# Performance work log

Measured on AMD Instinct MI355X. Metric: run time of the kernel, lower is better.

## Reference

```python
import jax, jax.numpy as jnp
import numpy as np

N_HEADS = 16
EMBED_DIM = 1024
HEAD_DIM = EMBED_DIM // N_HEADS
SRC_LEN = 128  # diagonal offset of the tril mask
B, T = 2, 2048


def setup_inputs() -> dict:
    key = jax.random.key(0)
    ks = jax.random.split(key, 7)
    s = 0.02
    return {
        "x": jax.random.normal(ks[0], (B, T, EMBED_DIM), dtype=jnp.float32),
        "Wq": jax.random.normal(ks[1], (EMBED_DIM, EMBED_DIM), dtype=jnp.float32) * s,
        "bq": jax.random.normal(ks[2], (EMBED_DIM,), dtype=jnp.float32) * s,
        "Wk": jax.random.normal(ks[3], (EMBED_DIM, EMBED_DIM), dtype=jnp.float32) * s,
        "bk": jax.random.normal(ks[4], (EMBED_DIM,), dtype=jnp.float32) * s,
        "Wv": jax.random.normal(ks[5], (EMBED_DIM, EMBED_DIM), dtype=jnp.float32) * s,
        "bv": jax.random.normal(ks[6], (EMBED_DIM,), dtype=jnp.float32) * s,
    }


def reference(x, Wq, bq, Wk, bk, Wv, bv):
    b, t, c = x.shape
    # project and split heads: [B, H, T, Dh]
    def heads(w, bias):
        y = x @ w.T + bias
        return y.reshape(b, t, N_HEADS, HEAD_DIM).transpose(0, 2, 1, 3)

    q = heads(Wq, bq)
    k = heads(Wk, bk)
    v = heads(Wv, bv)

    scale = HEAD_DIM ** -0.5
    attn = jnp.einsum("bhqd,bhkd->bhqk", q, k) * scale  # [B,H,T,T]
    # prefix-causal mask: key j allowed iff j <= i + SRC_LEN
    i = jnp.arange(t)[:, None]
    j = jnp.arange(t)[None, :]
    mask = j <= i + SRC_LEN  # [T, T]
    attn = jnp.where(mask[None, None], attn, -jnp.inf)
    attn = jax.nn.softmax(attn, axis=-1)
    # dropout p=0.0 -> identity in eval/reference
    out = jnp.einsum("bhqk,bhkd->bhqd", attn, v)  # [B,H,T,Dh]
    return out.transpose(0, 2, 1, 3).reshape(b, t, c)
```

## Files before the change

### kernel.cpp

```cpp
#include <hip/hip_runtime.h>
#include <hip/hip_bf16.h>

#define B_    2
#define T_    2048
#define C_    1024
#define H_    16
#define D_    64
#define SRCL_ 128

typedef short  short8 __attribute__((ext_vector_type(8)));
typedef float  f32x4  __attribute__((ext_vector_type(4)));
typedef unsigned short ushort4_t __attribute__((ext_vector_type(4)));
typedef unsigned int   uint4v    __attribute__((ext_vector_type(4)));

#define QSCALE 0.18033688011112042f

__device__ inline unsigned short f2bf(float f) {
    union { float f; unsigned u; } v; v.f = f;
    unsigned r = v.u + 0x7FFFu + ((v.u >> 16) & 1u);
    return (unsigned short)(r >> 16);
}

#if __has_builtin(__builtin_amdgcn_exp2f)
#define EXP2F(x) __builtin_amdgcn_exp2f(x)
#else
#define EXP2F(x) exp2f(x)
#endif

__device__ __forceinline__ void async_ld16(const void* g, void* l) {
    __builtin_amdgcn_global_load_lds(
        (const __attribute__((address_space(1))) unsigned int*)g,
        (__attribute__((address_space(3))) unsigned int*)l, 16, 0, 0);
}

__global__ __launch_bounds__(256) void convert_all(
        const float* __restrict__ x,
        const float* __restrict__ wq,
        const float* __restrict__ wk,
        const float* __restrict__ wv,
        unsigned short* __restrict__ xb,
        unsigned short* __restrict__ wb)
{
    const int NX = (B_ * T_ * C_) / 4;
    const int NW = (C_ * C_) / 4;
    int i = blockIdx.x * 256 + threadIdx.x;
    const float4* src;
    ushort4_t* dst;
    if (i < NX)               { src = (const float4*)x;  dst = (ushort4_t*)xb;                }
    else if (i < NX + NW)     { src = (const float4*)wq; dst = (ushort4_t*)wb;                i -= NX; }
    else if (i < NX + 2*NW)   { src = (const float4*)wk; dst = (ushort4_t*)(wb + C_*C_);      i -= NX + NW; }
    else                      { src = (const float4*)wv; dst = (ushort4_t*)(wb + 2*C_*C_);    i -= NX + 2*NW; }
    float4 v = src[i];
    ushort4_t o;
    o.x = f2bf(v.x); o.y = f2bf(v.y); o.z = f2bf(v.z); o.w = f2bf(v.w);
    dst[i] = o;
}

__global__ __launch_bounds__(512, 2) void gemm_qkv(
        const unsigned short* __restrict__ xb,
        const unsigned short* __restrict__ wb,
        const float* __restrict__ bq,
        const float* __restrict__ bk,
        const float* __restrict__ bv,
        unsigned short* __restrict__ qo,
        unsigned short* __restrict__ ktp,
        unsigned short* __restrict__ vtp)
{
    __shared__ __align__(16) unsigned short uni[65536];

    const int tid  = threadIdx.x;
    const int wave = tid >> 6;
    const int lane = tid & 63;
    const int lane15 = lane & 15;
    const int quad   = lane >> 4;
    const int wm = wave >> 2;
    const int wn = wave & 3;

    const int bid = blockIdx.x;
    const int xcd = bid & 7;
    const int jj  = bid >> 3;
    const int mt  = xcd * 2 + (jj / 12);
    const int nt  = jj % 12;
    const int m0 = mt * 256;
    const int n0 = nt * 256;

    f32x4 acc[8][4];
#pragma unroll
    for (int m = 0; m < 8; ++m)
#pragma unroll
        for (int n = 0; n < 4; ++n)
            acc[m][n] = (f32x4){0.f, 0.f, 0.f, 0.f};

    char* lds = (char*)uni;
    const unsigned short* gb = (wave < 4) ? (xb + (size_t)m0 * 1024)
                                          : (wb + (size_t)n0 * 1024);
    const unsigned short* gsrc =
        gb + ((wave & 3) * 64 + (lane >> 2)) * 1024 + (lane & 3) * 8;
    const int lbase0 = ((wave < 4) ? 0 : 32768) + (wave & 3) * 4096;

    auto stage = [&](int t2, int kk) {
        char* ld = lds + (t2 & 1) * 65536 + lbase0 + kk * 16384;
        const unsigned short* gs = gsrc + t2 * 64 + kk * 32;
        async_ld16(gs,             ld);
        async_ld16(gs + 16 * 1024, ld + 1024);
        async_ld16(gs + 32 * 1024, ld + 2048);
        async_ld16(gs + 48 * 1024, ld + 3072);
    };

    auto compute = [&](int cur, int kk) {
        const char* ab = lds + cur * 65536 + kk * 16384;
        const char* bb = ab + 32768;
        short8 a[8], b[4];
#pragma unroll
        for (int n = 0; n < 4; ++n)
            b[n] = *(const short8*)(bb + (wn * 64 + n * 16 + lane15) * 64 + quad * 16);
#pragma unroll
        for (int m = 0; m < 8; ++m)
            a[m] = *(const short8*)(ab + (wm * 128 + m * 16 + lane15) * 64 + quad * 16);
#pragma unroll
        for (int m = 0; m < 8; ++m)
#pragma unroll
            for (int n = 0; n < 4; ++n)
                acc[m][n] = __builtin_amdgcn_mfma_f32_16x16x32_bf16(a[m], b[n], acc[m][n], 0, 0, 0);
    };

    stage(0, 0);
    stage(0, 1);

    for (int t = 0; t < 16; ++t) {
        const int cur = t & 1;
        __asm__ volatile("s_waitcnt vmcnt(4)\n\ts_barrier" ::: "memory");
        if (t < 15) stage(t + 1, 0);
        compute(cur, 0);
        if (t < 15) {
            __asm__ volatile("s_waitcnt vmcnt(4)\n\ts_barrier" ::: "memory");
            stage(t + 1, 1);
        } else {
            __asm__ volatile("s_waitcnt vmcnt(0)\n\ts_barrier" ::: "memory");
        }
        compute(cur, 1);
    }

    __syncthreads();

    const int colbase = n0 + wn * 64;
    const int which   = colbase >> 10;
    const int jj0     = colbase & 1023;
    const int h       = jj0 >> 6;
    const float* bias_p = (which == 0 ? bq : (which == 1 ? bk : bv)) + jj0;
    const float oscale  = (which == 0) ? QSCALE : 1.0f;

    unsigned short* stg = &uni[wave * 4160];

#pragma unroll
    for (int pass = 0; pass < 2; ++pass) {
        if (which != 2) {
#pragma unroll
            for (int ni = 0; ni < 4; ++ni) {
                const float bias = bias_p[ni * 16 + lane15];
                const int d = ni * 16 + lane15;
                const int dbase = (d >> 3) * 520 + (d & 7);
#pragma unroll
                for (int mi = 0; mi < 4; ++mi)
#pragma unroll
                    for (int r = 0; r < 4; ++r) {
                        const int tt = mi * 16 + quad * 4 + r;
                        stg[dbase + tt * 8] =
                            f2bf((acc[pass * 4 + mi][ni][r] + bias) * oscale);
                    }
            }
        } else {
#pragma unroll
            for (int ni = 0; ni < 4; ++ni) {
                const float bias = bias_p[ni * 16 + lane15];
                const int d = ni * 16 + lane15;
#pragma unroll
                for (int mi = 0; mi < 4; ++mi)
#pragma unroll
                    for (int r = 0; r < 4; ++r) {
                        const int tt = mi * 16 + quad * 4 + r;
                        const int c  = ((tt >> 5) << 2) | ((tt >> 2) & 3);
                        const int s  = (((tt >> 4) & 1) << 2) | (tt & 3);
                        stg[c * 520 + d * 8 + s] =
                            f2bf(acc[pass * 4 + mi][ni][r] + bias);
                    }
            }
        }

        const int rowg = m0 + wm * 128 + pass * 64;
        const int bidx = rowg >> 11;
        const int t0   = rowg & 2047;
        const size_t bh = (size_t)bidx * H_ + h;
        unsigned short* gdst =
            (which == 0 ? qo : (which == 1 ? ktp : vtp))
            + bh * (size_t)(T_ * D_) + (t0 >> 6) * 4096;

#pragma unroll
        for (int c = 0; c < 8; ++c) {
            *(short8*)&gdst[(c * 64 + lane) * 8] = *(const short8*)&stg[c * 520 + lane * 8];
        }
    }
}

__global__ __launch_bounds__(256, 4) void attn(
        const unsigned short* __restrict__ qg,
        const unsigned short* __restrict__ kg,
        const unsigned short* __restrict__ vg,
        float* __restrict__ out)
{
    __shared__ __align__(16) unsigned short stage[2][8192];

    const int tid  = threadIdx.x;
    const int wave = tid >> 6;
    const int lane = tid & 63;
    const int lane15 = lane & 15;
    const int quad   = lane >> 4;

    const int bh = blockIdx.x & 31;
    const int a  = 31 - (blockIdx.x >> 5);
    const int b  = bh >> 4;
    const int h  = bh & 15;
    const int i0 = a * 64 + wave * 16;

    const unsigned short* Q  = qg + (size_t)bh * T_ * D_;
    const unsigned short* KT = kg + (size_t)bh * T_ * D_;
    const unsigned short* VT = vg + (size_t)bh * T_ * D_;

    const int qrow = wave * 16 + lane15;
    const short8 qf0 = *(const short8*)&Q[a * 4096 + quad * 512 + qrow * 8];
    const short8 qf1 = *(const short8*)&Q[a * 4096 + (4 + quad) * 512 + qrow * 8];

    f32x4 o_acc[4];
#pragma unroll
    for (int di = 0; di < 4; ++di) o_acc[di] = (f32x4){0.f, 0.f, 0.f, 0.f};
    float l_p = 0.f;

    const int ntiles = min(a + 3, 32);
    const int limit  = i0 + lane15 + SRCL_;

    const int ib = wave * 4;
    const int loff = lane * 8;

#pragma unroll
    for (int c = 0; c < 4; ++c) {
        const int i = ib + c;
        const unsigned short* src = (i < 8) ? &KT[i * 512 + loff]
                                            : &VT[(i - 8) * 512 + loff];
        async_ld16(src, &stage[0][i * 512]);
    }

    for (int it = 0; it < ntiles; ++it) {
        __asm__ volatile("s_waitcnt vmcnt(0)\n\ts_barrier" ::: "memory");

        if (it + 1 < ntiles) {
            unsigned short* nb = &stage[(it + 1) & 1][0];
            const size_t tb = (size_t)(it + 1) * 4096;
#pragma unroll
            for (int c = 0; c < 4; ++c) {
                const int i = ib + c;
                const unsigned short* src = (i < 8) ? &KT[tb + i * 512 + loff]
                                                    : &VT[tb + (i - 8) * 512 + loff];
                async_ld16(src, &nb[i * 512]);
            }
        }

        const unsigned short* sb = &stage[it & 1][0];
        const int j0 = it << 6;

        f32x4 sv[4];
#pragma unroll
        for (int ni = 0; ni < 4; ++ni) {
            const short8 kf0 = *(const short8*)&sb[quad * 512 + (ni * 16 + lane15) * 8];
            const short8 kf1 = *(const short8*)&sb[(4 + quad) * 512 + (ni * 16 + lane15) * 8];
            f32x4 t = (f32x4){0.f, 0.f, 0.f, 0.f};
            t = __builtin_amdgcn_mfma_f32_16x16x32_bf16(kf0, qf0, t, 0, 0, 0);
            t = __builtin_amdgcn_mfma_f32_16x16x32_bf16(kf1, qf1, t, 0, 0, 0);
            sv[ni] = t;
        }

        if (j0 + 63 > i0 + SRCL_) {
#pragma unroll
            for (int ni = 0; ni < 4; ++ni)
#pragma unroll
                for (int r = 0; r < 4; ++r) {
                    const int key = j0 + ni * 16 + quad * 4 + r;
                    if (key > limit) sv[ni][r] = -INFINITY;
                }
        }

        float lacc = 0.f;
        unsigned pw[8];
#pragma unroll
        for (int ni = 0; ni < 4; ++ni) {
            const float p0 = EXP2F(sv[ni][0]);
            const float p1 = EXP2F(sv[ni][1]);
            const float p2 = EXP2F(sv[ni][2]);
            const float p3 = EXP2F(sv[ni][3]);
            lacc += (p0 + p1) + (p2 + p3);
            const unsigned u0 = __float_as_uint(p0) + 0x8000u;
            const unsigned u1 = __float_as_uint(p1) + 0x8000u;
            const unsigned u2 = __float_as_uint(p2) + 0x8000u;
            const unsigned u3 = __float_as_uint(p3) + 0x8000u;
            pw[ni * 2]     = __builtin_amdgcn_perm(u1, u0, 0x07060302);
            pw[ni * 2 + 1] = __builtin_amdgcn_perm(u3, u2, 0x07060302);
        }
        l_p += lacc;

        const uint4v w0 = {pw[0], pw[1], pw[2], pw[3]};
        const uint4v w1 = {pw[4], pw[5], pw[6], pw[7]};
        const short8 pf0 = __builtin_bit_cast(short8, w0);
        const short8 pf1 = __builtin_bit_cast(short8, w1);

#pragma unroll
        for (int di = 0; di < 4; ++di) {
            const short8 vf0 = *(const short8*)&sb[4096 + quad * 512 + (di * 16 + lane15) * 8];
            const short8 vf1 = *(const short8*)&sb[4096 + (4 + quad) * 512 + (di * 16 + lane15) * 8];
            o_acc[di] = __builtin_amdgcn_mfma_f32_16x16x32_bf16(vf0, pf0, o_acc[di], 0, 0, 0);
            o_acc[di] = __builtin_amdgcn_mfma_f32_16x16x32_bf16(vf1, pf1, o_acc[di], 0, 0, 0);
        }
    }

    __syncthreads();

    float l0s = l_p + __shfl_xor(l_p, 16);
    const float inv = 1.0f / (l0s + __shfl_xor(l0s, 32));

    float* myOs = (float*)&stage[0][0] + wave * 2048;
#pragma unroll
    for (int di = 0; di < 4; ++di) {
        f32x4 v = o_acc[di] * inv;
        *(f32x4*)&myOs[lane15 * 68 + di * 16 + quad * 4] = v;
    }
    float* orow0 = out + ((size_t)(b * T_ + i0)) * C_ + h * 64;
#pragma unroll
    for (int c = 0; c < 4; ++c) {
        const int idx = c * 64 + lane;
        const int t   = idx >> 4;
        const int dc  = (idx & 15) * 4;
        float4 v = *(float4*)&myOs[t * 68 + dc];
        *(float4*)(orow0 + (size_t)t * C_ + dc) = v;
    }
}

extern "C" void kernel_launch(void* const* d_in, const int* in_sizes, int n_in,
                              void* d_out, int out_size, void* d_ws, size_t ws_size,
                              hipStream_t stream) {
    const float* x  = (const float*)d_in[0];
    const float* Wq = (const float*)d_in[1];
    const float* bq = (const float*)d_in[2];
    const float* Wk = (const float*)d_in[3];
    const float* bk = (const float*)d_in[4];
    const float* Wv = (const float*)d_in[5];
    const float* bv = (const float*)d_in[6];
    float* out = (float*)d_out;

    unsigned short* xb  = (unsigned short*)d_ws;
    unsigned short* wb  = xb  + (size_t)B_ * T_ * C_;
    unsigned short* qb  = wb  + (size_t)3 * C_ * C_;
    unsigned short* ktb = qb  + (size_t)B_ * H_ * T_ * D_;
    unsigned short* vtb = ktb + (size_t)B_ * H_ * T_ * D_;

    convert_all<<<7168, 256, 0, stream>>>(x, Wq, Wk, Wv, xb, wb);
    gemm_qkv<<<192, 512, 0, stream>>>(xb, wb, bq, bk, bv, qb, ktb, vtb);
    attn<<<1024, 256, 0, stream>>>(qb, ktb, vtb, out);
}
```

Baseline: 145.4 us.

## Restructure QKV GEMM mainloop with finer-grained staging, LDS swizzle and setprio

Measured after the change: 144.1 us. About the same (-0.8%).

```diff
diff --git a/kernel.cpp b/kernel.cpp
--- a/kernel.cpp
+++ b/kernel.cpp
@@ -91,54 +91,63 @@
         for (int n = 0; n < 4; ++n)
             acc[m][n] = (f32x4){0.f, 0.f, 0.f, 0.f};
 
-    char* lds = (char*)uni;
-    const unsigned short* gb = (wave < 4) ? (xb + (size_t)m0 * 1024)
-                                          : (wb + (size_t)n0 * 1024);
-    const unsigned short* gsrc =
-        gb + ((wave & 3) * 64 + (lane >> 2)) * 1024 + (lane & 3) * 8;
-    const int lbase0 = ((wave < 4) ? 0 : 32768) + (wave & 3) * 4096;
-
-    auto stage = [&](int t2, int kk) {
-        char* ld = lds + (t2 & 1) * 65536 + lbase0 + kk * 16384;
-        const unsigned short* gs = gsrc + t2 * 64 + kk * 32;
-        async_ld16(gs,             ld);
-        async_ld16(gs + 16 * 1024, ld + 1024);
-        async_ld16(gs + 32 * 1024, ld + 2048);
-        async_ld16(gs + 48 * 1024, ld + 3072);
+    const int srow  = tid >> 2;
+    const int kseg8 = ((tid & 3) ^ ((tid >> 3) & 3)) * 8;
+    const unsigned short* gA = xb + (size_t)(m0 + srow) * 1024 + kseg8;
+    const unsigned short* gB = wb + (size_t)(n0 + srow) * 1024 + kseg8;
+    char* lbase = (char*)uni + tid * 16;
+
+    auto stage = [&](int s) {
+        const int Tt = s >> 2, j = s & 3;
+        const unsigned short* g = ((j & 1) ? gB : gA) + Tt * 64 + (j >> 1) * 32;
+        char* l = lbase + (Tt & 1) * 65536 + (j & 1) * 32768 + (j >> 1) * 16384;
+        async_ld16(g, l);
+        async_ld16(g + 128 * 1024, l + 8192);
     };
 
-    auto compute = [&](int cur, int kk) {
-        const char* ab = lds + cur * 65536 + kk * 16384;
-        const char* bb = ab + 32768;
-        short8 a[8], b[4];
-#pragma unroll
-        for (int n = 0; n < 4; ++n)
-            b[n] = *(const short8*)(bb + (wn * 64 + n * 16 + lane15) * 64 + quad * 16);
-#pragma unroll
-        for (int m = 0; m < 8; ++m)
-            a[m] = *(const short8*)(ab + (wm * 128 + m * 16 + lane15) * 64 + quad * 16);
-#pragma unroll
-        for (int m = 0; m < 8; ++m)
-#pragma unroll
-            for (int n = 0; n < 4; ++n)
-                acc[m][n] = __builtin_amdgcn_mfma_f32_16x16x32_bf16(a[m], b[n], acc[m][n], 0, 0, 0);
-    };
-
-    stage(0, 0);
-    stage(0, 1);
-
-    for (int t = 0; t < 16; ++t) {
-        const int cur = t & 1;
-        __asm__ volatile("s_waitcnt vmcnt(4)\n\ts_barrier" ::: "memory");
-        if (t < 15) stage(t + 1, 0);
-        compute(cur, 0);
-        if (t < 15) {
-            __asm__ volatile("s_waitcnt vmcnt(4)\n\ts_barrier" ::: "memory");
-            stage(t + 1, 1);
-        } else {
-            __asm__ volatile("s_waitcnt vmcnt(0)\n\ts_barrier" ::: "memory");
-        }
-        compute(cur, 1);
+#pragma unroll
+    for (int s = 0; s < 6; ++s) stage(s);
+    __asm__ volatile("s_waitcnt vmcnt(4)\n\ts_barrier" ::: "memory");
+
+    const int swz = (quad ^ ((lane15 >> 1) & 3)) * 16;
+
+    for (int T = 0; T < 16; ++T) {
+        const char* bufp = (const char*)uni + (T & 1) * 65536;
+        short8 bf[4];
+#pragma unroll
+        for (int ph = 0; ph < 4; ++ph) {
+            const int h = ph & 1, kk = ph >> 1;
+            const char* Ap = bufp + kk * 16384;
+            const char* Bp = bufp + 32768 + kk * 16384;
+
+            short8 a[4];
+#pragma unroll
+            for (int mi = 0; mi < 4; ++mi)
+                a[mi] = *(const short8*)(Ap + (wm * 128 + h * 64 + mi * 16 + lane15) * 64 + swz);
+            if (h == 0) {
+#pragma unroll
+                for (int ni = 0; ni < 4; ++ni)
+                    bf[ni] = *(const short8*)(Bp + (wn * 64 + ni * 16 + lane15) * 64 + swz);
+            }
+
+            const int s = T * 4 + ph + 6;
+            if (s < 64) stage(s);
+
+            __asm__ volatile("s_barrier" ::: "memory");
+            __builtin_amdgcn_s_setprio(1);
+#pragma unroll
+            for (int mi = 0; mi < 4; ++mi)
+#pragma unroll
+                for (int ni = 0; ni < 4; ++ni)
+                    acc[h * 4 + mi][ni] = __builtin_amdgcn_mfma_f32_16x16x32_bf16(
+                        a[mi], bf[ni], acc[h * 4 + mi][ni], 0, 0, 0);
+            __builtin_amdgcn_s_setprio(0);
+
+            if (ph == 3)
+                __asm__ volatile("s_waitcnt vmcnt(4)\n\ts_barrier" ::: "memory");
+            else
+                __asm__ volatile("s_barrier" ::: "memory");
+        }
     }
 
     __syncthreads();
```
